# Kernel tuning notes

Measured on AMD Instinct MI355X. Metric: run time of the kernel, lower is better.

The kernel has to match this reference:

```python
import jax, jax.numpy as jnp
import numpy as np

BITS = 4
GROUP_SIZE = 128
IN_FEATURES = 4096
OUT_FEATURES = 11008
BATCH = 128


def setup_inputs() -> dict:
    key = jax.random.key(0)
    k1, k2, k3, k4 = jax.random.split(key, 4)
    x = jax.random.normal(k1, (BATCH, IN_FEATURES), dtype=jnp.float32)
    # packed 4-bit weights: each int32 holds 8 nibbles along the in-feature dim
    qweight = jax.random.randint(k2, (IN_FEATURES // 32 * BITS, OUT_FEATURES), 0, 2147483647, dtype=jnp.int32)
    n_groups = IN_FEATURES // GROUP_SIZE
    scales = jax.random.uniform(k3, (n_groups, OUT_FEATURES), dtype=jnp.float32) * 0.01 + 1e-3
    # note: in GPTQLinear_woo, `zeros` buffer already stores scale*zero_point
    zeros = jax.random.normal(k4, (n_groups, OUT_FEATURES), dtype=jnp.float32) * 0.01
    return {"x": x, "qweight": qweight, "scales": scales, "zeros": zeros}


def _dequant(qweight, scales, zeros):
    out_f = qweight.shape[1]
    shifts = jnp.arange(0, 32, BITS, dtype=jnp.int32)  # [8]
    # [in/8, 8, out] -> unpack nibbles (mask kills arithmetic-shift sign bits)
    w = (qweight[:, None, :] >> shifts[None, :, None]) & (2 ** BITS - 1)
    w = w.reshape(-1, GROUP_SIZE, out_f).astype(scales.dtype)  # [n_groups, gs, out]
    w = scales[:, None, :] * w - zeros[:, None, :]
    return w.reshape(-1, out_f)  # [in, out]


def reference(x, qweight, scales, zeros):
    w = _dequant(qweight, scales, zeros)
    return jnp.matmul(x, w)  # [batch, out]
```

## Files before the change

kernel.cpp:

```cpp
#include <hip/hip_runtime.h>
#include <hip/hip_bf16.h>
#include <stdint.h>


#define IN_F   4096
#define OUT_F  11008
#define BATCH  128
#define BK     64
#define BN     64
#define NCHUNK (IN_F / BK)
#define SPLIT  4
#define KSC    (NCHUNK / SPLIT)
#define NBLK   (OUT_F / BN)
#define MN     (BATCH * OUT_F)

typedef __attribute__((ext_vector_type(8))) short short8;
typedef __attribute__((ext_vector_type(4))) float f32x4;

static __device__ __forceinline__ unsigned int f2bf_pack(float lo, float hi) {
  unsigned int a = __float_as_uint(lo);
  unsigned int b = __float_as_uint(hi);
  a += 0x7FFFu + ((a >> 16) & 1u);
  b += 0x7FFFu + ((b >> 16) & 1u);
  return (a >> 16) | (b & 0xFFFF0000u);
}

__global__ __launch_bounds__(256) void cvt_kernel(const float* __restrict__ x,
                                                  unsigned int* __restrict__ xb) {
  int i = blockIdx.x * 256 + threadIdx.x;
  float4 v0 = *(const float4*)(x + (size_t)i * 8);
  float4 v1 = *(const float4*)(x + (size_t)i * 8 + 4);
  uint4 o;
  o.x = f2bf_pack(v0.x, v0.y);
  o.y = f2bf_pack(v0.z, v0.w);
  o.z = f2bf_pack(v1.x, v1.y);
  o.w = f2bf_pack(v1.z, v1.w);
  *(uint4*)(xb + (size_t)i * 4) = o;
}

__global__ __launch_bounds__(256) void zero_out(float* __restrict__ out) {
  int base = (blockIdx.x * 256 + threadIdx.x) * 16;
  float4 z = {0.f, 0.f, 0.f, 0.f};
#pragma unroll
  for (int j = 0; j < 4; ++j) *(float4*)(out + base + j * 4) = z;
}

__global__ __launch_bounds__(256) void reduce_kernel(const float* __restrict__ part,
                                                     float* __restrict__ out) {
  int base = (blockIdx.x * 256 + threadIdx.x) * 8;
  float4 s0 = {0.f, 0.f, 0.f, 0.f}, s1 = s0;
#pragma unroll
  for (int s = 0; s < SPLIT; ++s) {
    const float* p = part + (size_t)s * MN + base;
    float4 a = *(const float4*)(p);
    float4 b = *(const float4*)(p + 4);
    s0.x += a.x; s0.y += a.y; s0.z += a.z; s0.w += a.w;
    s1.x += b.x; s1.y += b.y; s1.z += b.z; s1.w += b.w;
  }
  *(float4*)(out + base)     = s0;
  *(float4*)(out + base + 4) = s1;
}

__global__ __launch_bounds__(256) void gptq_gemm(
    const unsigned short* __restrict__ xb,
    const float* __restrict__ x,
    const int* __restrict__ qweight,
    const float* __restrict__ scales,
    const float* __restrict__ zeros,
    float* __restrict__ outp,
    int use_xb, int atomic_mode) {
  __shared__ char aLds[BATCH * 128];
  __shared__ char bLds[BN * 128];

  const int tid  = threadIdx.x;
  const int lane = tid & 63;
  const int wid  = tid >> 6;
  const int wr   = wid >> 1;
  const int wc   = wid & 1;
  const int nb   = blockIdx.x % NBLK;
  const int sl   = blockIdx.x / NBLK;
  const int n0   = nb * BN;
  const int c0   = sl * KSC;

  float* dst = atomic_mode ? outp : outp + (size_t)sl * MN;

  const int col = tid & 63;
  const int g0  = c0 >> 1;
  float sreg[8], zreg[8];
#pragma unroll
  for (int g = 0; g < 8; ++g) {
    sreg[g] = scales[(size_t)(g0 + g) * OUT_F + n0 + col];
    zreg[g] = zeros [(size_t)(g0 + g) * OUT_F + n0 + col];
  }

  uint4 aPre[4];
  unsigned int qPre[2];

  {
    const int k0 = c0 * BK;
#pragma unroll
    for (int i = 0; i < 4; ++i) {
      int seg = tid + 256 * i, row = seg >> 3, sc2 = seg & 7;
      if (use_xb) {
        aPre[i] = *(const uint4*)(xb + (size_t)row * IN_F + k0 + sc2 * 8);
      } else {
        const float* p = x + (size_t)row * IN_F + k0 + sc2 * 8;
        float4 u0 = *(const float4*)(p);
        float4 u1 = *(const float4*)(p + 4);
        aPre[i].x = f2bf_pack(u0.x, u0.y);
        aPre[i].y = f2bf_pack(u0.z, u0.w);
        aPre[i].z = f2bf_pack(u1.x, u1.y);
        aPre[i].w = f2bf_pack(u1.z, u1.w);
      }
    }
#pragma unroll
    for (int i = 0; i < 2; ++i) {
      int qr = wid + 4 * i;
      qPre[i] = (unsigned int)qweight[(size_t)(k0 / 8 + qr) * OUT_F + n0 + col];
    }
  }

  f32x4 acc[4][2] = {};

  for (int cc = 0; cc < KSC; ++cc) {
    __syncthreads();

#pragma unroll
    for (int i = 0; i < 4; ++i) {
      int seg = tid + 256 * i, row = seg >> 3, sc2 = seg & 7;
      int off = row * 128 + ((sc2 * 16) ^ ((row & 7) << 4));
      *(uint4*)(aLds + off) = aPre[i];
    }

    {
      float s = sreg[cc >> 1];
      float z = zreg[cc >> 1];
#pragma unroll
      for (int i = 0; i < 2; ++i) {
        unsigned int q = qPre[i];
        int qr = wid + 4 * i;
        float f0 = s * (float)((q >> 0)  & 0xFu) - z;
        float f1 = s * (float)((q >> 4)  & 0xFu) - z;
        float f2 = s * (float)((q >> 8)  & 0xFu) - z;
        float f3 = s * (float)((q >> 12) & 0xFu) - z;
        float f4 = s * (float)((q >> 16) & 0xFu) - z;
        float f5 = s * (float)((q >> 20) & 0xFu) - z;
        float f6 = s * (float)((q >> 24) & 0xFu) - z;
        float f7 = s * (float)((q >> 28) & 0xFu) - z;
        uint4 v;
        v.x = f2bf_pack(f0, f1);
        v.y = f2bf_pack(f2, f3);
        v.z = f2bf_pack(f4, f5);
        v.w = f2bf_pack(f6, f7);
        int off = col * 128 + ((qr * 16) ^ ((col & 7) << 4));
        *(uint4*)(bLds + off) = v;
      }
    }
    __syncthreads();

    if (cc + 1 < KSC) {
      const int k0 = (c0 + cc + 1) * BK;
#pragma unroll
      for (int i = 0; i < 4; ++i) {
        int seg = tid + 256 * i, row = seg >> 3, sc2 = seg & 7;
        if (use_xb) {
          aPre[i] = *(const uint4*)(xb + (size_t)row * IN_F + k0 + sc2 * 8);
        } else {
          const float* p = x + (size_t)row * IN_F + k0 + sc2 * 8;
          float4 u0 = *(const float4*)(p);
          float4 u1 = *(const float4*)(p + 4);
          aPre[i].x = f2bf_pack(u0.x, u0.y);
          aPre[i].y = f2bf_pack(u0.z, u0.w);
          aPre[i].z = f2bf_pack(u1.x, u1.y);
          aPre[i].w = f2bf_pack(u1.z, u1.w);
        }
      }
#pragma unroll
      for (int i = 0; i < 2; ++i) {
        int qr = wid + 4 * i;
        qPre[i] = (unsigned int)qweight[(size_t)(k0 / 8 + qr) * OUT_F + n0 + col];
      }
    }

#pragma unroll
    for (int ks = 0; ks < 2; ++ks) {
      int kbyte = ks * 64 + ((lane >> 4) << 4);
      short8 bfrag[2];
#pragma unroll
      for (int ct = 0; ct < 2; ++ct) {
        int c = wc * 32 + ct * 16 + (lane & 15);
        bfrag[ct] = *(const short8*)(bLds + c * 128 + (kbyte ^ ((c & 7) << 4)));
      }
#pragma unroll
      for (int rt = 0; rt < 4; ++rt) {
        int row = wr * 64 + rt * 16 + (lane & 15);
        short8 afrag = *(const short8*)(aLds + row * 128 + (kbyte ^ ((row & 7) << 4)));
#pragma unroll
        for (int ct = 0; ct < 2; ++ct) {
          acc[rt][ct] = __builtin_amdgcn_mfma_f32_16x16x32_bf16(afrag, bfrag[ct], acc[rt][ct], 0, 0, 0);
        }
      }
    }
  }

#pragma unroll
  for (int rt = 0; rt < 4; ++rt) {
#pragma unroll
    for (int ct = 0; ct < 2; ++ct) {
      int c = n0 + wc * 32 + ct * 16 + (lane & 15);
#pragma unroll
      for (int r = 0; r < 4; ++r) {
        int row = wr * 64 + rt * 16 + ((lane >> 4) << 2) + r;
        if (atomic_mode) {
          atomicAdd(dst + (size_t)row * OUT_F + c, acc[rt][ct][r]);
        } else {
          dst[(size_t)row * OUT_F + c] = acc[rt][ct][r];
        }
      }
    }
  }
}

extern "C" void kernel_launch(void* const* d_in, const int* in_sizes, int n_in,
                              void* d_out, int out_size, void* d_ws, size_t ws_size,
                              hipStream_t stream) {
  const float* x       = (const float*)d_in[0];
  const int*   qweight = (const int*)d_in[1];
  const float* scales  = (const float*)d_in[2];
  const float* zeros   = (const float*)d_in[3];
  float*       outp    = (float*)d_out;

  const size_t xb_bytes   = (size_t)BATCH * IN_F * sizeof(unsigned short);
  const size_t part_bytes = (size_t)SPLIT * MN * sizeof(float);
  int use_xb   = (ws_size >= xb_bytes) ? 1 : 0;
  int partials = (ws_size >= xb_bytes + part_bytes) ? 1 : 0;

  unsigned short* xb   = (unsigned short*)d_ws;
  float*          part = (float*)((char*)d_ws + xb_bytes);

  if (use_xb) {
    cvt_kernel<<<256, 256, 0, stream>>>(x, (unsigned int*)d_ws);
  }

  if (partials) {
    gptq_gemm<<<NBLK * SPLIT, 256, 0, stream>>>(xb, x, qweight, scales, zeros,
                                                part, use_xb, 0);
    reduce_kernel<<<688, 256, 0, stream>>>(part, outp);
  } else {
    zero_out<<<344, 256, 0, stream>>>(outp);
    gptq_gemm<<<NBLK * SPLIT, 256, 0, stream>>>(xb, x, qweight, scales, zeros,
                                                outp, use_xb, 1);
  }
}
```

Measured before the change: 42.27 us.

## Double register prefetch two chunks ahead and raise split-K to eight

The main loop now keeps two register prefetch buffers and loads chunk cc+2 while chunk cc is staged into LDS. This deepens the global-load pipeline and hides more memory latency. SPLIT goes from 4 to 8, which doubles the grid (more blocks for the CUs) and halves the K chunks per block. In exchange, the partials buffer and the reduce pass double in size, and register pressure rises from the extra buffers and the fully unrolled loop.

```diff
diff --git a/kernel.cpp b/kernel.cpp
--- a/kernel.cpp
+++ b/kernel.cpp
@@ -9,7 +9,7 @@
 #define BK     64
 #define BN     64
 #define NCHUNK (IN_F / BK)
-#define SPLIT  4
+#define SPLIT  8
 #define KSC    (NCHUNK / SPLIT)
 #define NBLK   (OUT_F / BN)
 #define MN     (BATCH * OUT_F)
@@ -61,6 +61,60 @@
   *(float4*)(out + base + 4) = s1;
 }
 
+#define LOAD_CHUNK(AP, QP, CH) do {                                            \
+    const int k0_ = (CH) * BK;                                                 \
+    _Pragma("unroll")                                                          \
+    for (int i_ = 0; i_ < 4; ++i_) {                                           \
+      int seg_ = tid + 256 * i_, row_ = seg_ >> 3, sc_ = seg_ & 7;             \
+      if (use_xb) {                                                            \
+        AP[i_] = *(const uint4*)(xb + (size_t)row_ * IN_F + k0_ + sc_ * 8);    \
+      } else {                                                                 \
+        const float* p_ = x + (size_t)row_ * IN_F + k0_ + sc_ * 8;             \
+        float4 u0_ = *(const float4*)(p_);                                     \
+        float4 u1_ = *(const float4*)(p_ + 4);                                 \
+        AP[i_].x = f2bf_pack(u0_.x, u0_.y);                                    \
+        AP[i_].y = f2bf_pack(u0_.z, u0_.w);                                    \
+        AP[i_].z = f2bf_pack(u1_.x, u1_.y);                                    \
+        AP[i_].w = f2bf_pack(u1_.z, u1_.w);                                    \
+      }                                                                        \
+    }                                                                          \
+    _Pragma("unroll")                                                          \
+    for (int i_ = 0; i_ < 2; ++i_) {                                           \
+      QP[i_] = (unsigned int)qweight[(size_t)(k0_ / 8 + wid + 4 * i_) * OUT_F  \
+                                     + n0 + col];                              \
+    }                                                                          \
+  } while (0)
+
+#define STORE_CHUNK(AP, QP, CC) do {                                           \
+    _Pragma("unroll")                                                          \
+    for (int i_ = 0; i_ < 4; ++i_) {                                           \
+      int seg_ = tid + 256 * i_, row_ = seg_ >> 3, sc_ = seg_ & 7;             \
+      *(uint4*)(aLds + row_ * 128 + ((sc_ * 16) ^ ((row_ & 7) << 4))) = AP[i_];\
+    }                                                                          \
+    {                                                                          \
+      float s_ = sreg[(CC) >> 1], z_ = zreg[(CC) >> 1];                        \
+      _Pragma("unroll")                                                        \
+      for (int i_ = 0; i_ < 2; ++i_) {                                         \
+        unsigned int q_ = QP[i_];                                              \
+        int qr_ = wid + 4 * i_;                                                \
+        float f0_ = s_ * (float)((q_ >> 0)  & 0xFu) - z_;                      \
+        float f1_ = s_ * (float)((q_ >> 4)  & 0xFu) - z_;                      \
+        float f2_ = s_ * (float)((q_ >> 8)  & 0xFu) - z_;                      \
+        float f3_ = s_ * (float)((q_ >> 12) & 0xFu) - z_;                      \
+        float f4_ = s_ * (float)((q_ >> 16) & 0xFu) - z_;                      \
+        float f5_ = s_ * (float)((q_ >> 20) & 0xFu) - z_;                      \
+        float f6_ = s_ * (float)((q_ >> 24) & 0xFu) - z_;                      \
+        float f7_ = s_ * (float)((q_ >> 28) & 0xFu) - z_;                      \
+        uint4 v_;                                                              \
+        v_.x = f2bf_pack(f0_, f1_);                                            \
+        v_.y = f2bf_pack(f2_, f3_);                                            \
+        v_.z = f2bf_pack(f4_, f5_);                                            \
+        v_.w = f2bf_pack(f6_, f7_);                                            \
+        *(uint4*)(bLds + col * 128 + ((qr_ * 16) ^ ((col & 7) << 4))) = v_;    \
+      }                                                                        \
+    }                                                                          \
+  } while (0)
+
 __global__ __launch_bounds__(256) void gptq_gemm(
     const unsigned short* __restrict__ xb,
     const float* __restrict__ x,
@@ -86,101 +140,32 @@
 
   const int col = tid & 63;
   const int g0  = c0 >> 1;
-  float sreg[8], zreg[8];
-#pragma unroll
-  for (int g = 0; g < 8; ++g) {
+  float sreg[KSC / 2], zreg[KSC / 2];
+#pragma unroll
+  for (int g = 0; g < KSC / 2; ++g) {
     sreg[g] = scales[(size_t)(g0 + g) * OUT_F + n0 + col];
     zreg[g] = zeros [(size_t)(g0 + g) * OUT_F + n0 + col];
   }
 
-  uint4 aPre[4];
-  unsigned int qPre[2];
-
-  {
-    const int k0 = c0 * BK;
-#pragma unroll
-    for (int i = 0; i < 4; ++i) {
-      int seg = tid + 256 * i, row = seg >> 3, sc2 = seg & 7;
-      if (use_xb) {
-        aPre[i] = *(const uint4*)(xb + (size_t)row * IN_F + k0 + sc2 * 8);
-      } else {
-        const float* p = x + (size_t)row * IN_F + k0 + sc2 * 8;
-        float4 u0 = *(const float4*)(p);
-        float4 u1 = *(const float4*)(p + 4);
-        aPre[i].x = f2bf_pack(u0.x, u0.y);
-        aPre[i].y = f2bf_pack(u0.z, u0.w);
-        aPre[i].z = f2bf_pack(u1.x, u1.y);
-        aPre[i].w = f2bf_pack(u1.z, u1.w);
-      }
-    }
-#pragma unroll
-    for (int i = 0; i < 2; ++i) {
-      int qr = wid + 4 * i;
-      qPre[i] = (unsigned int)qweight[(size_t)(k0 / 8 + qr) * OUT_F + n0 + col];
-    }
-  }
+  uint4 aP0[4], aP1[4];
+  unsigned int qP0[2], qP1[2];
+  LOAD_CHUNK(aP0, qP0, c0);
+  LOAD_CHUNK(aP1, qP1, c0 + 1);
 
   f32x4 acc[4][2] = {};
 
+#pragma unroll
   for (int cc = 0; cc < KSC; ++cc) {
     __syncthreads();
 
-#pragma unroll
-    for (int i = 0; i < 4; ++i) {
-      int seg = tid + 256 * i, row = seg >> 3, sc2 = seg & 7;
-      int off = row * 128 + ((sc2 * 16) ^ ((row & 7) << 4));
-      *(uint4*)(aLds + off) = aPre[i];
-    }
-
-    {
-      float s = sreg[cc >> 1];
-      float z = zreg[cc >> 1];
-#pragma unroll
-      for (int i = 0; i < 2; ++i) {
-        unsigned int q = qPre[i];
-        int qr = wid + 4 * i;
-        float f0 = s * (float)((q >> 0)  & 0xFu) - z;
-        float f1 = s * (float)((q >> 4)  & 0xFu) - z;
-        float f2 = s * (float)((q >> 8)  & 0xFu) - z;
-        float f3 = s * (float)((q >> 12) & 0xFu) - z;
-        float f4 = s * (float)((q >> 16) & 0xFu) - z;
-        float f5 = s * (float)((q >> 20) & 0xFu) - z;
-        float f6 = s * (float)((q >> 24) & 0xFu) - z;
-        float f7 = s * (float)((q >> 28) & 0xFu) - z;
-        uint4 v;
-        v.x = f2bf_pack(f0, f1);
-        v.y = f2bf_pack(f2, f3);
-        v.z = f2bf_pack(f4, f5);
-        v.w = f2bf_pack(f6, f7);
-        int off = col * 128 + ((qr * 16) ^ ((col & 7) << 4));
-        *(uint4*)(bLds + off) = v;
-      }
+    if ((cc & 1) == 0) {
+      STORE_CHUNK(aP0, qP0, cc);
+      if (cc + 2 < KSC) LOAD_CHUNK(aP0, qP0, c0 + cc + 2);
+    } else {
+      STORE_CHUNK(aP1, qP1, cc);
+      if (cc + 2 < KSC) LOAD_CHUNK(aP1, qP1, c0 + cc + 2);
     }
     __syncthreads();
-
-    if (cc + 1 < KSC) {
-      const int k0 = (c0 + cc + 1) * BK;
-#pragma unroll
-      for (int i = 0; i < 4; ++i) {
-        int seg = tid + 256 * i, row = seg >> 3, sc2 = seg & 7;
-        if (use_xb) {
-          aPre[i] = *(const uint4*)(xb + (size_t)row * IN_F + k0 + sc2 * 8);
-        } else {
-          const float* p = x + (size_t)row * IN_F + k0 + sc2 * 8;
-          float4 u0 = *(const float4*)(p);
-          float4 u1 = *(const float4*)(p + 4);
-          aPre[i].x = f2bf_pack(u0.x, u0.y);
-          aPre[i].y = f2bf_pack(u0.z, u0.w);
-          aPre[i].z = f2bf_pack(u1.x, u1.y);
-          aPre[i].w = f2bf_pack(u1.z, u1.w);
-        }
-      }
-#pragma unroll
-      for (int i = 0; i < 2; ++i) {
-        int qr = wid + 4 * i;
-        qPre[i] = (unsigned int)qweight[(size_t)(k0 / 8 + qr) * OUT_F + n0 + col];
-      }
-    }
 
 #pragma unroll
     for (int ks = 0; ks < 2; ++ks) {
```

Measured after the change: 44.43 us. 1.05x slower.
